# Optimization experiments

Measured on AMD Instinct MI355X. Metric: run time of the kernel, lower is better.

## Reference

```python
import jax, jax.numpy as jnp
import numpy as np

DIM = 64   # flow dimension
HID = 8    # hidden_dim=[8]
B = 131072 # batch of samples


def setup_inputs() -> dict:
    key = jax.random.key(0)
    ks = jax.random.split(key, 6)
    L = DIM - 1  # number of per-dim MLPs (layers[0..L-1], layer l has fan-in l+1)
    lim = float(np.sqrt(0.5))
    x = jax.random.normal(ks[0], (B, DIM), jnp.float32)
    initial_param = jax.random.uniform(ks[1], (2,), jnp.float32, -lim, lim)
    # Ragged Linear(fan_in=l+1, 8) weights stacked into padded [L, HID, L];
    # entries beyond column l are masked to zero in reference().
    fan_in = np.arange(1, DIM).astype(np.float32)          # (L,)
    bnd1 = (1.0 / np.sqrt(fan_in))[:, None, None]          # torch Linear default init bound
    W1 = jax.random.uniform(ks[2], (L, HID, L), jnp.float32, -1.0, 1.0) * bnd1
    b1 = jax.random.uniform(ks[3], (L, HID), jnp.float32, -1.0, 1.0) * bnd1[:, :, 0]
    bnd2 = 1.0 / np.sqrt(HID)
    W2 = jax.random.uniform(ks[4], (L, 2, HID), jnp.float32, -bnd2, bnd2)
    b2 = jax.random.uniform(ks[5], (L, 2), jnp.float32, -bnd2, bnd2)
    return {"x": x, "initial_param": initial_param, "W1": W1, "b1": b1, "W2": W2, "b2": b2}


def reference(x, initial_param, W1, b1, W2, b2):
    B_, D = x.shape
    L = W1.shape[0]  # D - 1
    # mask[l, d] = 1 iff d <= l  ->  layer l sees exactly x[:, :l+1]
    mask = jnp.tril(jnp.ones((L, L), x.dtype))
    W1m = W1 * mask[:, None, :]
    # all dim-1 tiny MLPs fused into two batched contractions
    h = jnp.tanh(jnp.einsum('bd,lhd->blh', x[:, :L], W1m) + b1)   # [B, L, HID]
    out = jnp.einsum('blh,loh->blo', h, W2) + b2                   # [B, L, 2]
    mu0 = jnp.broadcast_to(initial_param[0], (B_, 1)).astype(x.dtype)
    al0 = jnp.broadcast_to(initial_param[1], (B_, 1)).astype(x.dtype)
    mu = jnp.concatenate([mu0, out[:, :, 0]], axis=1)              # [B, D]
    alpha = jnp.concatenate([al0, out[:, :, 1]], axis=1)           # [B, D]
    z = x * jnp.exp(alpha) + mu
    log_det = jnp.sum(alpha, axis=1)
    return z, log_det
```

## Files before the change

kernel.cpp:

```cpp
#include <hip/hip_runtime.h>


#define DIMS 64
#define TPB  512
#define WAVES 8
#define SPW  16

typedef __attribute__((ext_vector_type(8))) short short8;
typedef __attribute__((ext_vector_type(4))) float f32x4;
typedef __attribute__((ext_vector_type(4))) unsigned int uint4v;
typedef unsigned short ushort_t;
typedef unsigned int uint_t;

#if __has_builtin(__builtin_amdgcn_exp2f)
#define YSCALE 2.8853900817779268f
#define EXP2F(x) __builtin_amdgcn_exp2f(x)
#else
#define YSCALE 2.8853900817779268f
#define EXP2F(x) exp2f(x)
#endif
#define LOG2E 1.4426950408889634f
#define LN2   0.6931471805599453f

#define A_OFF 0
#define BLO_OFF 16384
#define BHI_OFF 32768
#define C_OFF 49152
#define WT_BYTES 55808
#define CDE_BYTES 6656
#define PREP_N (24576 + 1664)

#define XZ_OFF CDE_BYTES
#define LDS_BYTES (CDE_BYTES + WAVES * SPW * DIMS * 4)

__device__ __align__(16) unsigned char g_ws[WT_BYTES];

__device__ __forceinline__ uint_t pk2bf(float a, float b) {
#if __has_builtin(__builtin_amdgcn_cvt_pk_bf16_f32)
    typedef __attribute__((ext_vector_type(2))) __bf16 bf16x2;
    bf16x2 r = __builtin_amdgcn_cvt_pk_bf16_f32(a, b);
    return __builtin_bit_cast(uint_t, r);
#else
    uint_t ua = __float_as_uint(a); ua += 0x7FFFu + ((ua >> 16) & 1u);
    uint_t ub = __float_as_uint(b); ub += 0x7FFFu + ((ub >> 16) & 1u);
    return (ub & 0xFFFF0000u) | (ua >> 16);
#endif
}

__device__ __forceinline__ ushort_t f2bf(float f) {
    uint_t u = __float_as_uint(f);
    u += 0x7FFFu + ((u >> 16) & 1u);
    return (ushort_t)(u >> 16);
}

__device__ __forceinline__ int logrow(int p) {
    int n = p & 15;
    return (p >> 5) * 32 + (n >> 2) * 8 + ((p >> 4) & 1) * 4 + (n & 3);
}

__global__ void siaf_prep(const float* __restrict__ W1, const float* __restrict__ b1,
                          const float* __restrict__ W2, const float* __restrict__ b2) {
    ushort_t* __restrict__ ws_u = (ushort_t*)g_ws;
    int i = blockIdx.x * 256 + threadIdx.x;
    if (i < 8192) {
        int p = i >> 5, k = i & 31;
        int L = logrow(p), l = L >> 3, h = L & 7;
        float v = (k <= l) ? W1[(l * 8 + h) * 63 + k] * YSCALE : 0.0f;
        ws_u[i] = f2bf(v);
    } else if (i < 16384) {
        int r = i - 8192;
        int p = 256 + (r >> 5), k = r & 31;
        int L = logrow(p), l = L >> 3, h = L & 7;
        float v = (l < 63 && k <= l) ? W1[(l * 8 + h) * 63 + k] * YSCALE : 0.0f;
        ws_u[i] = f2bf(v);
    } else if (i < 24576) {
        int r = i - 16384;
        int p = 256 + (r >> 5), k = 32 + (r & 31);
        int L = logrow(p), l = L >> 3, h = L & 7;
        float v = (l < 63 && k <= l) ? W1[(l * 8 + h) * 63 + k] * YSCALE : 0.0f;
        ws_u[i] = f2bf(v);
    } else if (i < PREP_N) {
        int f = i - 24576;
        float* fws = (float*)(g_ws + C_OFF);
        float v = 0.0f;
        if (f < 1024) {
            int l = f >> 4, o = (f >> 3) & 1, h = f & 7;
            if (l < 63) {
                v = -2.0f * W2[(l * 2 + o) * 8 + h];
                if (o) v *= LOG2E;
            }
        } else if (f < 1536) {
            int p = f - 1024;
            int L = logrow(p), l = L >> 3, h = L & 7;
            if (l < 63) v = b1[l * 8 + h] * YSCALE;
        } else {
            int j = f - 1536, l = j >> 1, o = j & 1;
            if (l < 63) {
                float s = b2[l * 2 + o];
                #pragma unroll
                for (int h = 0; h < 8; ++h) s += W2[(l * 2 + o) * 8 + h];
                v = o ? s * LOG2E : s;
            }
        }
        fws[f] = v;
    }
}

__device__ __forceinline__ float sg(float t) {
    float e = EXP2F(t);
    return __builtin_amdgcn_rcpf(e + 1.0f);
}

__global__ __launch_bounds__(TPB, 4) void siaf_main(
        const float* __restrict__ x, const float* __restrict__ ip,
        float* __restrict__ out, int nB) {
    extern __shared__ unsigned char lds[];

    const int tid  = threadIdx.x;
    const int wv   = tid >> 6, lane = tid & 63;
    const int s16  = lane & 15, quad = lane >> 4;
    const int sbase = blockIdx.x * (WAVES * SPW) + wv * SPW;
    float* xzw = (float*)(lds + XZ_OFF) + wv * (SPW * DIMS);

    #pragma unroll
    for (int g = 0; g < 4; ++g) {
        const float4 v = ((const float4*)(x + (size_t)sbase * DIMS))[g * 64 + lane];
        const int s_loc = 4 * g + quad;
        const int pc = (s16 ^ s_loc) & 15;
        *(float4*)(xzw + s_loc * 64 + pc * 4) = v;
    }
    const float ip0 = ip[0];
    const float ip1l2 = ip[1] * LOG2E;

    if (tid < CDE_BYTES / 16) {
        ((uint4*)lds)[tid] = ((const uint4*)(g_ws + C_OFF))[tid];
    }

    short8 bfr[2];
    #pragma unroll
    for (int kh = 0; kh < 2; ++kh) {
        const int c0 = kh * 8 + quad * 2;
        float4 va = *(const float4*)(xzw + s16 * 64 + ((c0 ^ s16) & 15) * 4);
        float4 vb = *(const float4*)(xzw + s16 * 64 + (((c0 + 1) ^ s16) & 15) * 4);
        uint4v u = {pk2bf(va.x, va.y), pk2bf(va.z, va.w),
                    pk2bf(vb.x, vb.y), pk2bf(vb.z, vb.w)};
        bfr[kh] = __builtin_bit_cast(short8, u);
    }

    __syncthreads();

    const float* w2f = (const float*)(lds);
    const float* b1f = (const float*)(lds + 4096);
    const float* b2f = (const float*)(lds + 6144);

    const ushort_t* gA   = (const ushort_t*)g_ws;
    const ushort_t* gBlo = (const ushort_t*)(g_ws + BLO_OFF);
    const ushort_t* gBhi = (const ushort_t*)(g_ws + BHI_OFF);
    const int fo = s16 * 32 + quad * 8;

    auto ldA = [&](int w, short8& a00, short8& a10, short8& a01, short8& a11) {
        if (w < 8) {
            const ushort_t* b = gA + w * 1024 + fo;
            a00 = *(const short8*)(b);
            a10 = *(const short8*)(b + 512);
        } else {
            const int off = (w - 8) * 1024 + fo;
            a00 = *(const short8*)(gBlo + off);
            a10 = *(const short8*)(gBlo + off + 512);
            a01 = *(const short8*)(gBhi + off);
            a11 = *(const short8*)(gBhi + off + 512);
        }
    };

    short8 A00[2], A10[2], A01[2] = {}, A11[2] = {};
    ldA(0, A00[0], A10[0], A01[0], A11[0]);
    ldA(1, A00[1], A10[1], A01[1], A11[1]);

    float lsum = 0.0f;
    #pragma unroll
    for (int w = 0; w < 16; ++w) {
        const int cur = w & 1;

        const float4 bi0 = *(const float4*)(b1f + w * 32 + quad * 4);
        const float4 bi1 = *(const float4*)(b1f + w * 32 + 16 + quad * 4);

        f32x4 aE = {bi0.x, bi0.y, bi0.z, bi0.w};
        f32x4 aO = {bi1.x, bi1.y, bi1.z, bi1.w};
        aE = __builtin_amdgcn_mfma_f32_16x16x32_bf16(A00[cur], bfr[0], aE, 0, 0, 0);
        aO = __builtin_amdgcn_mfma_f32_16x16x32_bf16(A10[cur], bfr[0], aO, 0, 0, 0);
        if (w >= 8) {
            aE = __builtin_amdgcn_mfma_f32_16x16x32_bf16(A01[cur], bfr[1], aE, 0, 0, 0);
            aO = __builtin_amdgcn_mfma_f32_16x16x32_bf16(A11[cur], bfr[1], aO, 0, 0, 0);
        }

        if (w < 14) ldA(w + 2, A00[cur], A10[cur], A01[cur], A11[cur]);

        const float r0 = sg(aE[0]), r1 = sg(aE[1]), r2 = sg(aE[2]), r3 = sg(aE[3]);
        const float r4 = sg(aO[0]), r5 = sg(aO[1]), r6 = sg(aO[2]), r7 = sg(aO[3]);

        const int l = 4 * w + quad;
        const float4 m0 = *(const float4*)(w2f + l * 16);
        const float4 m1 = *(const float4*)(w2f + l * 16 + 4);
        const float4 a0 = *(const float4*)(w2f + l * 16 + 8);
        const float4 a1 = *(const float4*)(w2f + l * 16 + 12);
        const float2 bb = *(const float2*)(b2f + l * 2);

        float mu0 = bb.x, mu1 = m1.x * r4;
        mu0 = fmaf(m0.x, r0, mu0); mu1 = fmaf(m1.y, r5, mu1);
        mu0 = fmaf(m0.y, r1, mu0); mu1 = fmaf(m1.z, r6, mu1);
        mu0 = fmaf(m0.z, r2, mu0); mu1 = fmaf(m1.w, r7, mu1);
        mu0 = fmaf(m0.w, r3, mu0);
        float mu = mu0 + mu1;
        float al0 = bb.y, al1 = a1.x * r4;
        al0 = fmaf(a0.x, r0, al0); al1 = fmaf(a1.y, r5, al1);
        al0 = fmaf(a0.y, r1, al0); al1 = fmaf(a1.z, r6, al1);
        al0 = fmaf(a0.z, r2, al0); al1 = fmaf(a1.w, r7, al1);
        al0 = fmaf(a0.w, r3, al0);
        float alg = al0 + al1;

        int d = l + 1;
        if (w == 15) {
            const bool pad = (quad == 3);
            alg = pad ? ip1l2 : alg;
            mu  = pad ? ip0 : mu;
            d   = pad ? 0 : d;
        }
        float* pz = xzw + s16 * 64 + ((((d >> 2) ^ s16) & 15) << 2) + (d & 3);
        *pz = fmaf(*pz, EXP2F(alg), mu);
        lsum += alg;
    }

    #pragma unroll
    for (int g = 0; g < 4; ++g) {
        const int s_loc = 4 * g + quad;
        const int pc = (s16 ^ s_loc) & 15;
        const float4 v = *(const float4*)(xzw + s_loc * 64 + pc * 4);
        ((float4*)(out + (size_t)sbase * DIMS))[g * 64 + lane] = v;
    }

    {
        float v = lsum;
        int r1 = __builtin_amdgcn_ds_swizzle(__float_as_int(v), 0x401F);
        v += __int_as_float(r1);
        int r2 = __builtin_amdgcn_ds_bpermute((lane ^ 32) << 2, __float_as_int(v));
        v += __int_as_float(r2);
        if (quad == 0)
            out[(size_t)nB * DIMS + sbase + s16] = v * LN2;
    }
}

extern "C" void kernel_launch(void* const* d_in, const int* in_sizes, int n_in,
                              void* d_out, int out_size, void* d_ws, size_t ws_size,
                              hipStream_t stream) {
    const float* x  = (const float*)d_in[0];
    const float* ip = (const float*)d_in[1];
    const float* W1 = (const float*)d_in[2];
    const float* b1 = (const float*)d_in[3];
    const float* W2 = (const float*)d_in[4];
    const float* b2 = (const float*)d_in[5];
    float* out = (float*)d_out;
    (void)d_ws; (void)ws_size;

    const int nB = in_sizes[0] / DIMS;
    const int grid = nB / (WAVES * SPW);

    (void)hipFuncSetAttribute((const void*)siaf_main,
                              hipFuncAttributeMaxDynamicSharedMemorySize, LDS_BYTES);

    siaf_prep<<<(PREP_N + 255) / 256, 256, 0, stream>>>(W1, b1, W2, b2);
    siaf_main<<<grid, TPB, LDS_BYTES, stream>>>(x, ip, out, nB);
}
```

Before: 114.2 us.

## Process two 16-sample groups per wave to reuse A-fragment loads

Each wave now handles 32 samples instead of 16. Every weight fragment loaded from global memory feeds two MFMA sets, one per 16-sample group, so per-sample weight loads are halved and there is more independent work to overlap. The explicit double-buffered prefetch of A fragments is dropped in favour of plain loads inside the unrolled loop. In exchange, LDS use per block doubles, the grid halves, and register pressure rises, which may lower occupancy and leave load latency exposed.

```diff
diff --git a/kernel.cpp b/kernel.cpp
--- a/kernel.cpp
+++ b/kernel.cpp
@@ -4,7 +4,7 @@
 #define DIMS 64
 #define TPB  512
 #define WAVES 8
-#define SPW  16
+#define SPW  32
 
 typedef __attribute__((ext_vector_type(8))) short short8;
 typedef __attribute__((ext_vector_type(4))) float f32x4;
@@ -123,7 +123,7 @@
     float* xzw = (float*)(lds + XZ_OFF) + wv * (SPW * DIMS);
 
     #pragma unroll
-    for (int g = 0; g < 4; ++g) {
+    for (int g = 0; g < 8; ++g) {
         const float4 v = ((const float4*)(x + (size_t)sbase * DIMS))[g * 64 + lane];
         const int s_loc = 4 * g + quad;
         const int pc = (s16 ^ s_loc) & 15;
@@ -136,15 +136,19 @@
         ((uint4*)lds)[tid] = ((const uint4*)(g_ws + C_OFF))[tid];
     }
 
-    short8 bfr[2];
-    #pragma unroll
-    for (int kh = 0; kh < 2; ++kh) {
-        const int c0 = kh * 8 + quad * 2;
-        float4 va = *(const float4*)(xzw + s16 * 64 + ((c0 ^ s16) & 15) * 4);
-        float4 vb = *(const float4*)(xzw + s16 * 64 + (((c0 + 1) ^ s16) & 15) * 4);
-        uint4v u = {pk2bf(va.x, va.y), pk2bf(va.z, va.w),
-                    pk2bf(vb.x, vb.y), pk2bf(vb.z, vb.w)};
-        bfr[kh] = __builtin_bit_cast(short8, u);
+    short8 bfA[2], bfB[2];
+    #pragma unroll
+    for (int grp = 0; grp < 2; ++grp) {
+        const int s = s16 + 16 * grp;
+        #pragma unroll
+        for (int kh = 0; kh < 2; ++kh) {
+            const int c0 = kh * 8 + quad * 2;
+            float4 va = *(const float4*)(xzw + s * 64 + ((c0 ^ s) & 15) * 4);
+            float4 vb = *(const float4*)(xzw + s * 64 + (((c0 + 1) ^ s) & 15) * 4);
+            uint4v u = {pk2bf(va.x, va.y), pk2bf(va.z, va.w),
+                        pk2bf(vb.x, vb.y), pk2bf(vb.z, vb.w)};
+            (grp ? bfB : bfA)[kh] = __builtin_bit_cast(short8, u);
+        }
     }
 
     __syncthreads();
@@ -158,7 +162,10 @@
     const ushort_t* gBhi = (const ushort_t*)(g_ws + BHI_OFF);
     const int fo = s16 * 32 + quad * 8;
 
-    auto ldA = [&](int w, short8& a00, short8& a10, short8& a01, short8& a11) {
+    float lsA = 0.0f, lsB = 0.0f;
+    #pragma unroll
+    for (int w = 0; w < 16; ++w) {
+        short8 a00, a10, a01{}, a11{};
         if (w < 8) {
             const ushort_t* b = gA + w * 1024 + fo;
             a00 = *(const short8*)(b);
@@ -170,33 +177,23 @@
             a01 = *(const short8*)(gBhi + off);
             a11 = *(const short8*)(gBhi + off + 512);
         }
-    };
-
-    short8 A00[2], A10[2], A01[2] = {}, A11[2] = {};
-    ldA(0, A00[0], A10[0], A01[0], A11[0]);
-    ldA(1, A00[1], A10[1], A01[1], A11[1]);
-
-    float lsum = 0.0f;
-    #pragma unroll
-    for (int w = 0; w < 16; ++w) {
-        const int cur = w & 1;
 
         const float4 bi0 = *(const float4*)(b1f + w * 32 + quad * 4);
         const float4 bi1 = *(const float4*)(b1f + w * 32 + 16 + quad * 4);
 
-        f32x4 aE = {bi0.x, bi0.y, bi0.z, bi0.w};
-        f32x4 aO = {bi1.x, bi1.y, bi1.z, bi1.w};
-        aE = __builtin_amdgcn_mfma_f32_16x16x32_bf16(A00[cur], bfr[0], aE, 0, 0, 0);
-        aO = __builtin_amdgcn_mfma_f32_16x16x32_bf16(A10[cur], bfr[0], aO, 0, 0, 0);
+        f32x4 aEa = {bi0.x, bi0.y, bi0.z, bi0.w};
+        f32x4 aOa = {bi1.x, bi1.y, bi1.z, bi1.w};
+        f32x4 aEb = aEa, aOb = aOa;
+        aEa = __builtin_amdgcn_mfma_f32_16x16x32_bf16(a00, bfA[0], aEa, 0, 0, 0);
+        aEb = __builtin_amdgcn_mfma_f32_16x16x32_bf16(a00, bfB[0], aEb, 0, 0, 0);
+        aOa = __builtin_amdgcn_mfma_f32_16x16x32_bf16(a10, bfA[0], aOa, 0, 0, 0);
+        aOb = __builtin_amdgcn_mfma_f32_16x16x32_bf16(a10, bfB[0], aOb, 0, 0, 0);
         if (w >= 8) {
-            aE = __builtin_amdgcn_mfma_f32_16x16x32_bf16(A01[cur], bfr[1], aE, 0, 0, 0);
-            aO = __builtin_amdgcn_mfma_f32_16x16x32_bf16(A11[cur], bfr[1], aO, 0, 0, 0);
-        }
-
-        if (w < 14) ldA(w + 2, A00[cur], A10[cur], A01[cur], A11[cur]);
-
-        const float r0 = sg(aE[0]), r1 = sg(aE[1]), r2 = sg(aE[2]), r3 = sg(aE[3]);
-        const float r4 = sg(aO[0]), r5 = sg(aO[1]), r6 = sg(aO[2]), r7 = sg(aO[3]);
+            aEa = __builtin_amdgcn_mfma_f32_16x16x32_bf16(a01, bfA[1], aEa, 0, 0, 0);
+            aEb = __builtin_amdgcn_mfma_f32_16x16x32_bf16(a01, bfB[1], aEb, 0, 0, 0);
+            aOa = __builtin_amdgcn_mfma_f32_16x16x32_bf16(a11, bfA[1], aOa, 0, 0, 0);
+            aOb = __builtin_amdgcn_mfma_f32_16x16x32_bf16(a11, bfB[1], aOb, 0, 0, 0);
+        }
 
         const int l = 4 * w + quad;
         const float4 m0 = *(const float4*)(w2f + l * 16);
@@ -205,33 +202,43 @@
         const float4 a1 = *(const float4*)(w2f + l * 16 + 12);
         const float2 bb = *(const float2*)(b2f + l * 2);
 
-        float mu0 = bb.x, mu1 = m1.x * r4;
-        mu0 = fmaf(m0.x, r0, mu0); mu1 = fmaf(m1.y, r5, mu1);
-        mu0 = fmaf(m0.y, r1, mu0); mu1 = fmaf(m1.z, r6, mu1);
-        mu0 = fmaf(m0.z, r2, mu0); mu1 = fmaf(m1.w, r7, mu1);
-        mu0 = fmaf(m0.w, r3, mu0);
-        float mu = mu0 + mu1;
-        float al0 = bb.y, al1 = a1.x * r4;
-        al0 = fmaf(a0.x, r0, al0); al1 = fmaf(a1.y, r5, al1);
-        al0 = fmaf(a0.y, r1, al0); al1 = fmaf(a1.z, r6, al1);
-        al0 = fmaf(a0.z, r2, al0); al1 = fmaf(a1.w, r7, al1);
-        al0 = fmaf(a0.w, r3, al0);
-        float alg = al0 + al1;
-
-        int d = l + 1;
-        if (w == 15) {
-            const bool pad = (quad == 3);
-            alg = pad ? ip1l2 : alg;
-            mu  = pad ? ip0 : mu;
-            d   = pad ? 0 : d;
-        }
-        float* pz = xzw + s16 * 64 + ((((d >> 2) ^ s16) & 15) << 2) + (d & 3);
-        *pz = fmaf(*pz, EXP2F(alg), mu);
-        lsum += alg;
-    }
-
-    #pragma unroll
-    for (int g = 0; g < 4; ++g) {
+        #pragma unroll
+        for (int grp = 0; grp < 2; ++grp) {
+            const f32x4 aE = grp ? aEb : aEa;
+            const f32x4 aO = grp ? aOb : aOa;
+            const int s = s16 + 16 * grp;
+
+            const float r0 = sg(aE[0]), r1 = sg(aE[1]), r2 = sg(aE[2]), r3 = sg(aE[3]);
+            const float r4 = sg(aO[0]), r5 = sg(aO[1]), r6 = sg(aO[2]), r7 = sg(aO[3]);
+
+            float mu0 = bb.x, mu1 = m1.x * r4;
+            mu0 = fmaf(m0.x, r0, mu0); mu1 = fmaf(m1.y, r5, mu1);
+            mu0 = fmaf(m0.y, r1, mu0); mu1 = fmaf(m1.z, r6, mu1);
+            mu0 = fmaf(m0.z, r2, mu0); mu1 = fmaf(m1.w, r7, mu1);
+            mu0 = fmaf(m0.w, r3, mu0);
+            float mu = mu0 + mu1;
+            float al0 = bb.y, al1 = a1.x * r4;
+            al0 = fmaf(a0.x, r0, al0); al1 = fmaf(a1.y, r5, al1);
+            al0 = fmaf(a0.y, r1, al0); al1 = fmaf(a1.z, r6, al1);
+            al0 = fmaf(a0.z, r2, al0); al1 = fmaf(a1.w, r7, al1);
+            al0 = fmaf(a0.w, r3, al0);
+            float alg = al0 + al1;
+
+            int d = l + 1;
+            if (w == 15) {
+                const bool pad = (quad == 3);
+                alg = pad ? ip1l2 : alg;
+                mu  = pad ? ip0 : mu;
+                d   = pad ? 0 : d;
+            }
+            float* pz = xzw + s * 64 + ((((d >> 2) ^ s) & 15) << 2) + (d & 3);
+            *pz = fmaf(*pz, EXP2F(alg), mu);
+            if (grp) lsB += alg; else lsA += alg;
+        }
+    }
+
+    #pragma unroll
+    for (int g = 0; g < 8; ++g) {
         const int s_loc = 4 * g + quad;
         const int pc = (s16 ^ s_loc) & 15;
         const float4 v = *(const float4*)(xzw + s_loc * 64 + pc * 4);
@@ -239,13 +246,19 @@
     }
 
     {
-        float v = lsum;
-        int r1 = __builtin_amdgcn_ds_swizzle(__float_as_int(v), 0x401F);
-        v += __int_as_float(r1);
-        int r2 = __builtin_amdgcn_ds_bpermute((lane ^ 32) << 2, __float_as_int(v));
-        v += __int_as_float(r2);
-        if (quad == 0)
-            out[(size_t)nB * DIMS + sbase + s16] = v * LN2;
+        float va = lsA, vb = lsB;
+        int r1a = __builtin_amdgcn_ds_swizzle(__float_as_int(va), 0x401F);
+        int r1b = __builtin_amdgcn_ds_swizzle(__float_as_int(vb), 0x401F);
+        va += __int_as_float(r1a);
+        vb += __int_as_float(r1b);
+        int r2a = __builtin_amdgcn_ds_bpermute((lane ^ 32) << 2, __float_as_int(va));
+        int r2b = __builtin_amdgcn_ds_bpermute((lane ^ 32) << 2, __float_as_int(vb));
+        va += __int_as_float(r2a);
+        vb += __int_as_float(r2b);
+        if (quad == 0) {
+            out[(size_t)nB * DIMS + sbase + s16] = va * LN2;
+            out[(size_t)nB * DIMS + sbase + 16 + s16] = vb * LN2;
+        }
     }
 }
 
```

After: 110.4 us. 1.03x faster.
